# Optimization experiments

Measured on AMD Instinct MI355X. Metric: run time of the kernel, lower is better.

The kernel has to match this reference:

```python
import jax, jax.numpy as jnp
import numpy as np

B, N, E = 2, 20000, 200000
IN_F, OUT_F, HEADS = 256, 32, 4
NEG_SLOPE = 0.2


def setup_inputs() -> dict:
    key = jax.random.key(0)
    k1, k2, k3, k4 = jax.random.split(key, 4)
    x = jax.random.normal(k1, (B, N, IN_F), dtype=jnp.float32)
    edge_indices = jax.random.randint(k2, (2, E), 0, N, dtype=jnp.int64)
    # xavier-uniform-like scales
    W = jax.random.normal(k3, (OUT_F * HEADS, IN_F), dtype=jnp.float32) * np.float32(1.0 / np.sqrt(IN_F))
    a = jax.random.normal(k4, (2 * OUT_F, 1), dtype=jnp.float32) * np.float32(0.1)
    return {"x": x, "edge_indices": edge_indices, "W": W, "a": a}


def reference(x, edge_indices, W, a):
    Bq, Nq, _ = x.shape
    Hh, Ff = HEADS, OUT_F
    # h: [B, N, H, F]
    h = (x @ W.T).reshape(Bq, Nq, Hh, Ff)
    src, dst = edge_indices[0], edge_indices[1]
    Eq = src.shape[0]
    h_src = h[:, src]  # [B, E, H, F]
    h_dst = h[:, dst]  # [B, E, H, F]
    # scores = leaky_relu(concat(h_src, h_dst) @ a)  without materializing concat
    a_src, a_dst = a[:Ff, 0], a[Ff:, 0]
    scores = (jnp.einsum('behf,f->beh', h_src, a_src)
              + jnp.einsum('behf,f->beh', h_dst, a_dst))
    scores = jnp.where(scores > 0, scores, NEG_SLOPE * scores)  # LeakyReLU(0.2)
    # Original applies softmax over dim=0 (the BATCH dim) per edge
    sm = jax.nn.softmax(scores, axis=0)  # [B, E, H]
    # Original loop overwrites attention_weights[:, src] per edge, so only the
    # LAST edge with a given src survives.
    edge_ids = jnp.arange(Eq, dtype=jnp.int32)
    last_edge = jax.ops.segment_max(edge_ids, src, num_segments=Nq)
    has_edge = jax.ops.segment_sum(jnp.ones((Eq,), jnp.int32), src, num_segments=Nq) > 0
    last_edge = jnp.clip(last_edge, 0, Eq - 1)
    aw = jnp.where(has_edge[None, :, None], sm[:, last_edge], 0.0)  # [B, N, H]
    # aggregated[:, s] = aw[:, s] * sum_{edges i: src[i]==s} h_dst[:, i]
    seg = jax.ops.segment_sum(jnp.transpose(h_dst, (1, 0, 2, 3)), src, num_segments=Nq)  # [N,B,H,F]
    seg = jnp.transpose(seg, (1, 0, 2, 3))  # [B, N, H, F]
    aggregated = aw[..., None] * seg
    # mean over heads; dropout is identity in eval mode
    return aggregated.mean(axis=2)  # [B, N, F]
```

## Files before the change

kernel.cpp:

```cpp
#include <hip/hip_runtime.h>
#include <hip/hip_bf16.h>

#define BB 2
#define NN 20000
#define EE 200000
#define INF 256
#define OUTF 32
#define NH 4
#define HF 128
#define NEG_SLOPE 0.2f
#define GEMM_BLOCKS 625
#define EDGE_BLOCKS 782
#define CAP 96
#define OVF_CAP 8192

using bf16 = __hip_bfloat16;
typedef __attribute__((ext_vector_type(8))) short bf16x8;
typedef __attribute__((ext_vector_type(4))) float f32x4;

__device__ __forceinline__ float bf2f(unsigned short s){ return __uint_as_float((unsigned)s << 16); }
__device__ __forceinline__ ushort f2bf_bits(float f){
    __hip_bfloat16 b = __float2bfloat16(f);
    return *(ushort*)&b;
}

__device__ __forceinline__ int get_src(const int* ei, int e, int f64){
    return f64 ? ei[2 * e] : ei[e];
}
__device__ __forceinline__ int get_dst(const int* ei, int e, int f64){
    return f64 ? ei[2 * EE + 2 * e] : ei[EE + e];
}

__global__ void k_init(const ushort* __restrict__ xr, const int* __restrict__ er,
                       const void* __restrict__ Wv,
                       int* __restrict__ flags, ushort* __restrict__ wbf,
                       int* __restrict__ cnt, int* __restrict__ last_e,
                       int* __restrict__ ovf_cnt){
    int i = blockIdx.x * blockDim.x + threadIdx.x;
    if (i < NN){ cnt[i] = 0; last_e[i] = -1; }
    if (i == 0) *ovf_cnt = 0;
    if (blockIdx.x < 16){
        __shared__ int cnt_big, cnt_nz;
        if (threadIdx.x == 0){ cnt_big = 0; cnt_nz = 0; }
        __syncthreads();
        int big = 0;
        for (int k = threadIdx.x; k < 8192; k += blockDim.x){
            unsigned e = ((unsigned)xr[2 * k] >> 7) & 0xff;
            if (e >= 0xC0) big++;
        }
        int nz = 0;
        for (int k = threadIdx.x; k < 4096; k += blockDim.x){
            if (er[2 * k + 1] != 0) nz++;
        }
        atomicAdd(&cnt_big, big);
        atomicAdd(&cnt_nz, nz);
        __syncthreads();
        if (blockIdx.x == 0 && threadIdx.x == 0){
            flags[0] = (cnt_big >= 16) ? 1 : 0;
            flags[1] = (cnt_nz == 0) ? 1 : 0;
        }
        const bool f32w = (cnt_big >= 16);
        int fr = blockIdx.x * 256 + threadIdx.x;
        {
            int lane = fr & 63;
            int t    = (fr >> 6) & 3;
            int kc   = (fr >> 8) & 7;
            int ch   = fr >> 11;
            int col  = ch * 64 + t * 16 + (lane & 15);
            int kb   = kc * 32 + (lane >> 4) * 8;
            bf16x8 v;
            if (f32w){
                const float* wg = (const float*)Wv + (size_t)col * INF + kb;
                #pragma unroll
                for (int j = 0; j < 8; ++j) v[j] = (short)f2bf_bits(wg[j]);
            } else {
                const ushort* wg = (const ushort*)Wv + (size_t)col * INF + kb;
                #pragma unroll
                for (int j = 0; j < 8; ++j) v[j] = (short)wg[j];
            }
            *(bf16x8*)(wbf + (size_t)fr * 8) = v;
        }
    }
}

__global__ __launch_bounds__(256, 2)
void k_gemm(const void* __restrict__ xv_, const ushort* __restrict__ wbf,
            const void* __restrict__ av, const int* __restrict__ ei,
            const int* __restrict__ flags, ushort* __restrict__ h,
            float* __restrict__ alpha_s, float* __restrict__ alpha_d,
            int* __restrict__ last_e, int* __restrict__ cnt,
            ushort* __restrict__ slots, int* __restrict__ ovf_cnt,
            int* __restrict__ ovf_list){
    if (blockIdx.x < EDGE_BLOCKS){
        int f64 = flags[1];
        int e = blockIdx.x * 256 + threadIdx.x;
        if (e < EE){
            int s = get_src(ei, e, f64);
            int d = get_dst(ei, e, f64);
            atomicMax(&last_e[s], e);
            int idx = atomicAdd(&cnt[s], 1);
            if (idx < CAP) slots[(size_t)s * CAP + idx] = (ushort)d;
            else { int o = atomicAdd(ovf_cnt, 1); if (o < OVF_CAP) ovf_list[o] = e; }
        }
        return;
    }

    const int bid  = blockIdx.x - EDGE_BLOCKS;
    const int tid  = threadIdx.x;
    const int lane = tid & 63;
    const int w    = tid >> 6;
    const int l15  = lane & 15;
    const int q    = lane >> 4;
    const bool f32 = flags[0] != 0;

    const int row0 = bid * 64 + w * 16;

    f32x4 acc[2][4];
    #pragma unroll
    for (int c = 0; c < 2; ++c)
        #pragma unroll
        for (int t = 0; t < 4; ++t) acc[c][t] = (f32x4){0.f, 0.f, 0.f, 0.f};

    if (f32){
        const float* xp = (const float*)xv_ + (size_t)(row0 + l15) * INF + q * 8;
        float4 c0 = ((const float4*)xp)[0];
        float4 c1 = ((const float4*)xp)[1];
        #pragma unroll
        for (int kc = 0; kc < 8; ++kc){
            float4 n0, n1;
            if (kc < 7){
                const float4* p = (const float4*)(xp + (kc + 1) * 32);
                n0 = p[0];
                n1 = p[1];
            }
            bf16x8 afrag;
            afrag[0] = (short)f2bf_bits(c0.x); afrag[1] = (short)f2bf_bits(c0.y);
            afrag[2] = (short)f2bf_bits(c0.z); afrag[3] = (short)f2bf_bits(c0.w);
            afrag[4] = (short)f2bf_bits(c1.x); afrag[5] = (short)f2bf_bits(c1.y);
            afrag[6] = (short)f2bf_bits(c1.z); afrag[7] = (short)f2bf_bits(c1.w);
            #pragma unroll
            for (int c = 0; c < 2; ++c){
                const ushort* wb = wbf + (size_t)c * 16384;
                #pragma unroll
                for (int t = 0; t < 4; ++t){
                    bf16x8 bfrag = *(const bf16x8*)(wb + (((size_t)kc * 4 + t) * 64 + lane) * 8);
                    acc[c][t] = __builtin_amdgcn_mfma_f32_16x16x32_bf16(afrag, bfrag, acc[c][t], 0, 0, 0);
                }
            }
            if (kc < 7){ c0 = n0; c1 = n1; }
        }
    } else {
        const ushort* xp = (const ushort*)xv_ + (size_t)(row0 + l15) * INF + q * 8;
        bf16x8 af = *(const bf16x8*)xp;
        #pragma unroll
        for (int kc = 0; kc < 8; ++kc){
            bf16x8 nf;
            if (kc < 7) nf = *(const bf16x8*)(xp + (kc + 1) * 32);
            #pragma unroll
            for (int c = 0; c < 2; ++c){
                const ushort* wb = wbf + (size_t)c * 16384;
                #pragma unroll
                for (int t = 0; t < 4; ++t){
                    bf16x8 bfrag = *(const bf16x8*)(wb + (((size_t)kc * 4 + t) * 64 + lane) * 8);
                    acc[c][t] = __builtin_amdgcn_mfma_f32_16x16x32_bf16(af, bfrag, acc[c][t], 0, 0, 0);
                }
            }
            if (kc < 7) af = nf;
        }
    }

    #pragma unroll
    for (int r = 0; r < 4; ++r){
        int row = row0 + q * 4 + r;
        #pragma unroll
        for (int t = 0; t < 2; ++t){
            unsigned v0 = (unsigned)f2bf_bits(acc[0][t][r])
                        | ((unsigned)f2bf_bits(acc[0][t + 2][r]) << 16);
            unsigned v1 = (unsigned)f2bf_bits(acc[1][t][r])
                        | ((unsigned)f2bf_bits(acc[1][t + 2][r]) << 16);
            int f = t * 16 + l15;
            uint2 vv; vv.x = v0; vv.y = v1;
            *(uint2*)(h + (size_t)row * HF + f * 4) = vv;
        }
    }

    float as_lo, as_hi, ad_lo, ad_hi;
    if (f32){
        const float* af = (const float*)av;
        as_lo = af[l15];        as_hi = af[16 + l15];
        ad_lo = af[OUTF + l15]; ad_hi = af[OUTF + 16 + l15];
    } else {
        const ushort* ab = (const ushort*)av;
        as_lo = bf2f(ab[l15]);        as_hi = bf2f(ab[16 + l15]);
        ad_lo = bf2f(ab[OUTF + l15]); ad_hi = bf2f(ab[OUTF + 16 + l15]);
    }
    #pragma unroll
    for (int r = 0; r < 4; ++r){
        int row = row0 + q * 4 + r;
        #pragma unroll
        for (int c = 0; c < 2; ++c){
            #pragma unroll
            for (int hp = 0; hp < 2; ++hp){
                int t0 = hp * 2, t1 = hp * 2 + 1;
                float ps = acc[c][t0][r] * as_lo + acc[c][t1][r] * as_hi;
                float pd = acc[c][t0][r] * ad_lo + acc[c][t1][r] * ad_hi;
                ps += __shfl_down(ps, 8, 16); pd += __shfl_down(pd, 8, 16);
                ps += __shfl_down(ps, 4, 16); pd += __shfl_down(pd, 4, 16);
                ps += __shfl_down(ps, 2, 16); pd += __shfl_down(pd, 2, 16);
                ps += __shfl_down(ps, 1, 16); pd += __shfl_down(pd, 1, 16);
                if (l15 == 0){
                    size_t o = (size_t)row * NH + c * 2 + hp;
                    alpha_s[o] = ps;
                    alpha_d[o] = pd;
                }
            }
        }
    }
}

__global__ __launch_bounds__(256)
void k_agg(const ushort* __restrict__ slots, const int* __restrict__ cnt,
           const int* __restrict__ last_e, const int* __restrict__ ei,
           const int* __restrict__ flags,
           const float* __restrict__ alpha_s, const float* __restrict__ alpha_d,
           const ushort* __restrict__ h, float* __restrict__ aw,
           float* __restrict__ out_f){
    int lane = threadIdx.x & 63;
    int wid  = (blockIdx.x * blockDim.x + threadIdx.x) >> 6;
    int nw   = (gridDim.x * blockDim.x) >> 6;
    int b = lane >> 5;
    int f = lane & 31;
    int c  = lane & 7;
    int bb = c >> 2;
    int hh = c & 3;
    int f64 = flags[1];
    for (int n = wid; n < NN; n += nw){
        int m  = cnt[n]; if (m > CAP) m = CAP;
        int le = last_e[n];

        float my_aw = 0.f;
        if (le >= 0){
            int d = get_dst(ei, le, f64);
            float ss = alpha_s[((size_t)bb * NN + n) * NH + hh]
                     + alpha_d[((size_t)bb * NN + d) * NH + hh];
            float so = alpha_s[((size_t)(1 - bb) * NN + n) * NH + hh]
                     + alpha_d[((size_t)(1 - bb) * NN + d) * NH + hh];
            ss = ss > 0.f ? ss : NEG_SLOPE * ss;
            so = so > 0.f ? so : NEG_SLOPE * so;
            float mx = fmaxf(ss, so);
            float e0 = __expf(ss - mx);
            float e1 = __expf(so - mx);
            my_aw = 0.25f * e0 / (e0 + e1);
        }
        if (lane < 8) aw[((size_t)bb * NN + n) * NH + hh] = my_aw;

        float aw0 = __shfl(my_aw, (b << 2) + 0, 8);
        float aw1 = __shfl(my_aw, (b << 2) + 1, 8);
        float aw2 = __shfl(my_aw, (b << 2) + 2, 8);
        float aw3 = __shfl(my_aw, (b << 2) + 3, 8);

        const ushort* sl = slots + (size_t)n * CAP;
        const ushort* hb = h + (size_t)b * NN * HF + f * 4;
        float ax = 0.f, ay = 0.f, az = 0.f, aww = 0.f;
        int i = 0;
        for (; i + 4 <= m; i += 4){
            ushort4 dd = *(const ushort4*)(sl + i);
            ushort4 u0 = *(const ushort4*)(hb + (size_t)dd.x * HF);
            ushort4 u1 = *(const ushort4*)(hb + (size_t)dd.y * HF);
            ushort4 u2 = *(const ushort4*)(hb + (size_t)dd.z * HF);
            ushort4 u3 = *(const ushort4*)(hb + (size_t)dd.w * HF);
            ax += bf2f(u0.x) + bf2f(u1.x) + bf2f(u2.x) + bf2f(u3.x);
            ay += bf2f(u0.y) + bf2f(u1.y) + bf2f(u2.y) + bf2f(u3.y);
            az += bf2f(u0.z) + bf2f(u1.z) + bf2f(u2.z) + bf2f(u3.z);
            aww += bf2f(u0.w) + bf2f(u1.w) + bf2f(u2.w) + bf2f(u3.w);
        }
        for (; i < m; ++i){
            ushort4 u = *(const ushort4*)(hb + (size_t)sl[i] * HF);
            ax += bf2f(u.x); ay += bf2f(u.y); az += bf2f(u.z); aww += bf2f(u.w);
        }
        out_f[((size_t)b * NN + n) * OUTF + f] =
            aw0 * ax + aw1 * ay + aw2 * az + aw3 * aww;
    }
}

__global__ void k_fix(const int* __restrict__ ei, const int* __restrict__ flags,
                      const int* __restrict__ ovf_cnt, const int* __restrict__ ovf_list,
                      const ushort* __restrict__ h, const float* __restrict__ aw,
                      float* __restrict__ out_f){
    int lane = threadIdx.x & 63;
    int wid  = (blockIdx.x * blockDim.x + threadIdx.x) >> 6;
    int nw   = (gridDim.x * blockDim.x) >> 6;
    int b = lane >> 5;
    int f = lane & 31;
    int M = *ovf_cnt; if (M > OVF_CAP) M = OVF_CAP;
    int f64 = flags[1];
    for (int i = wid; i < M; i += nw){
        int e = ovf_list[i];
        int s = get_src(ei, e, f64);
        int d = get_dst(ei, e, f64);
        float4 awv = *(const float4*)(aw + ((size_t)b * NN + s) * NH);
        ushort4 u = *(const ushort4*)(h + ((size_t)b * NN + d) * HF + f * 4);
        float acc = awv.x * bf2f(u.x) + awv.y * bf2f(u.y)
                  + awv.z * bf2f(u.z) + awv.w * bf2f(u.w);
        atomicAdd(&out_f[((size_t)b * NN + s) * OUTF + f], acc);
    }
}

extern "C" void kernel_launch(void* const* d_in, const int* in_sizes, int n_in,
                              void* d_out, int out_size, void* d_ws, size_t ws_size,
                              hipStream_t stream){
    const void* x = d_in[0]; const void* eiv = d_in[1];
    const void* W = d_in[2]; const void* a  = d_in[3];
    for (int i = 0; i < n_in; ++i){
        if      (in_sizes[i] == BB * NN * INF) x   = d_in[i];
        else if (in_sizes[i] == 2 * EE)        eiv = d_in[i];
        else if (in_sizes[i] == HF * INF)      W   = d_in[i];
        else if (in_sizes[i] == 2 * OUTF)      a   = d_in[i];
    }
    const int* ei = (const int*)eiv;
    float* out = (float*)d_out;

    const size_t HN = (size_t)BB * NN * HF;
    char* p = (char*)d_ws;
    int*    flags    = (int*)p;                       p += 64;
    ushort* wbf      = (ushort*)p;                    p += 32768 * 2;
    ushort* h        = (ushort*)p;                    p += HN * 2;
    float*  alpha_s  = (float*)p;                     p += (size_t)BB * NN * NH * 4;
    float*  alpha_d  = (float*)p;                     p += (size_t)BB * NN * NH * 4;
    float*  aw       = (float*)p;                     p += (size_t)BB * NN * NH * 4;
    int*    last_e   = (int*)p;                       p += (size_t)NN * 4;
    int*    cnt      = (int*)p;                       p += (size_t)NN * 4;
    int*    ovf_cnt  = (int*)p;                       p += 64;
    int*    ovf_list = (int*)p;                       p += (size_t)OVF_CAP * 4;
    ushort* slots    = (ushort*)p;

    k_init <<<(NN + 255) / 256, 256, 0, stream>>>((const ushort*)x, ei, W, flags, wbf,
                                                  cnt, last_e, ovf_cnt);
    k_gemm <<<EDGE_BLOCKS + GEMM_BLOCKS, 256, 0, stream>>>(x, wbf, a, ei, flags, h,
                                                           alpha_s, alpha_d, last_e,
                                                           cnt, slots, ovf_cnt, ovf_list);
    k_agg  <<<2048, 256, 0, stream>>>(slots, cnt, last_e, ei, flags,
                                      alpha_s, alpha_d, h, aw, out);
    k_fix  <<<32, 256, 0, stream>>>(ei, flags, ovf_cnt, ovf_list, h, aw, out);
}
```

Before: 153.6 us.

## Store edge ids in slots and derive last edge during aggregation

```diff
diff --git a/kernel.cpp b/kernel.cpp
--- a/kernel.cpp
+++ b/kernel.cpp
@@ -11,7 +11,7 @@
 #define NEG_SLOPE 0.2f
 #define GEMM_BLOCKS 625
 #define EDGE_BLOCKS 782
-#define CAP 96
+#define CAP 48
 #define OVF_CAP 8192
 
 using bf16 = __hip_bfloat16;
@@ -89,18 +89,20 @@
             const int* __restrict__ flags, ushort* __restrict__ h,
             float* __restrict__ alpha_s, float* __restrict__ alpha_d,
             int* __restrict__ last_e, int* __restrict__ cnt,
-            ushort* __restrict__ slots, int* __restrict__ ovf_cnt,
+            unsigned* __restrict__ slots, int* __restrict__ ovf_cnt,
             int* __restrict__ ovf_list){
     if (blockIdx.x < EDGE_BLOCKS){
         int f64 = flags[1];
         int e = blockIdx.x * 256 + threadIdx.x;
         if (e < EE){
             int s = get_src(ei, e, f64);
-            int d = get_dst(ei, e, f64);
-            atomicMax(&last_e[s], e);
             int idx = atomicAdd(&cnt[s], 1);
-            if (idx < CAP) slots[(size_t)s * CAP + idx] = (ushort)d;
-            else { int o = atomicAdd(ovf_cnt, 1); if (o < OVF_CAP) ovf_list[o] = e; }
+            if (idx < CAP) slots[(size_t)s * CAP + idx] = (unsigned)e;
+            else {
+                atomicMax(&last_e[s], e);
+                int o = atomicAdd(ovf_cnt, 1);
+                if (o < OVF_CAP) ovf_list[o] = e;
+            }
         }
         return;
     }
@@ -219,7 +221,7 @@
 }
 
 __global__ __launch_bounds__(256)
-void k_agg(const ushort* __restrict__ slots, const int* __restrict__ cnt,
+void k_agg(const unsigned* __restrict__ slots, const int* __restrict__ cnt,
            const int* __restrict__ last_e, const int* __restrict__ ei,
            const int* __restrict__ flags,
            const float* __restrict__ alpha_s, const float* __restrict__ alpha_d,
@@ -238,6 +240,35 @@
         int m  = cnt[n]; if (m > CAP) m = CAP;
         int le = last_e[n];
 
+        const unsigned* sl = slots + (size_t)n * CAP;
+        const ushort* hb = h + (size_t)b * NN * HF + f * 4;
+        float ax = 0.f, ay = 0.f, az = 0.f, aww = 0.f;
+        int i = 0;
+        for (; i + 4 <= m; i += 4){
+            uint4 ee = *(const uint4*)(sl + i);
+            le = max(le, (int)ee.x); le = max(le, (int)ee.y);
+            le = max(le, (int)ee.z); le = max(le, (int)ee.w);
+            int d0 = get_dst(ei, (int)ee.x, f64);
+            int d1 = get_dst(ei, (int)ee.y, f64);
+            int d2 = get_dst(ei, (int)ee.z, f64);
+            int d3 = get_dst(ei, (int)ee.w, f64);
+            ushort4 u0 = *(const ushort4*)(hb + (size_t)d0 * HF);
+            ushort4 u1 = *(const ushort4*)(hb + (size_t)d1 * HF);
+            ushort4 u2 = *(const ushort4*)(hb + (size_t)d2 * HF);
+            ushort4 u3 = *(const ushort4*)(hb + (size_t)d3 * HF);
+            ax += bf2f(u0.x) + bf2f(u1.x) + bf2f(u2.x) + bf2f(u3.x);
+            ay += bf2f(u0.y) + bf2f(u1.y) + bf2f(u2.y) + bf2f(u3.y);
+            az += bf2f(u0.z) + bf2f(u1.z) + bf2f(u2.z) + bf2f(u3.z);
+            aww += bf2f(u0.w) + bf2f(u1.w) + bf2f(u2.w) + bf2f(u3.w);
+        }
+        for (; i < m; ++i){
+            int e = (int)sl[i];
+            le = max(le, e);
+            int d = get_dst(ei, e, f64);
+            ushort4 u = *(const ushort4*)(hb + (size_t)d * HF);
+            ax += bf2f(u.x); ay += bf2f(u.y); az += bf2f(u.z); aww += bf2f(u.w);
+        }
+
         float my_aw = 0.f;
         if (le >= 0){
             int d = get_dst(ei, le, f64);
@@ -259,25 +290,6 @@
         float aw2 = __shfl(my_aw, (b << 2) + 2, 8);
         float aw3 = __shfl(my_aw, (b << 2) + 3, 8);
 
-        const ushort* sl = slots + (size_t)n * CAP;
-        const ushort* hb = h + (size_t)b * NN * HF + f * 4;
-        float ax = 0.f, ay = 0.f, az = 0.f, aww = 0.f;
-        int i = 0;
-        for (; i + 4 <= m; i += 4){
-            ushort4 dd = *(const ushort4*)(sl + i);
-            ushort4 u0 = *(const ushort4*)(hb + (size_t)dd.x * HF);
-            ushort4 u1 = *(const ushort4*)(hb + (size_t)dd.y * HF);
-            ushort4 u2 = *(const ushort4*)(hb + (size_t)dd.z * HF);
-            ushort4 u3 = *(const ushort4*)(hb + (size_t)dd.w * HF);
-            ax += bf2f(u0.x) + bf2f(u1.x) + bf2f(u2.x) + bf2f(u3.x);
-            ay += bf2f(u0.y) + bf2f(u1.y) + bf2f(u2.y) + bf2f(u3.y);
-            az += bf2f(u0.z) + bf2f(u1.z) + bf2f(u2.z) + bf2f(u3.z);
-            aww += bf2f(u0.w) + bf2f(u1.w) + bf2f(u2.w) + bf2f(u3.w);
-        }
-        for (; i < m; ++i){
-            ushort4 u = *(const ushort4*)(hb + (size_t)sl[i] * HF);
-            ax += bf2f(u.x); ay += bf2f(u.y); az += bf2f(u.z); aww += bf2f(u.w);
-        }
         out_f[((size_t)b * NN + n) * OUTF + f] =
             aw0 * ax + aw1 * ay + aw2 * az + aw3 * aww;
     }
@@ -322,17 +334,17 @@
 
     const size_t HN = (size_t)BB * NN * HF;
     char* p = (char*)d_ws;
-    int*    flags    = (int*)p;                       p += 64;
-    ushort* wbf      = (ushort*)p;                    p += 32768 * 2;
-    ushort* h        = (ushort*)p;                    p += HN * 2;
-    float*  alpha_s  = (float*)p;                     p += (size_t)BB * NN * NH * 4;
-    float*  alpha_d  = (float*)p;                     p += (size_t)BB * NN * NH * 4;
-    float*  aw       = (float*)p;                     p += (size_t)BB * NN * NH * 4;
-    int*    last_e   = (int*)p;                       p += (size_t)NN * 4;
-    int*    cnt      = (int*)p;                       p += (size_t)NN * 4;
-    int*    ovf_cnt  = (int*)p;                       p += 64;
-    int*    ovf_list = (int*)p;                       p += (size_t)OVF_CAP * 4;
-    ushort* slots    = (ushort*)p;
+    int*      flags    = (int*)p;                     p += 64;
+    ushort*   wbf      = (ushort*)p;                  p += 32768 * 2;
+    ushort*   h        = (ushort*)p;                  p += HN * 2;
+    float*    alpha_s  = (float*)p;                   p += (size_t)BB * NN * NH * 4;
+    float*    alpha_d  = (float*)p;                   p += (size_t)BB * NN * NH * 4;
+    float*    aw       = (float*)p;                   p += (size_t)BB * NN * NH * 4;
+    int*      last_e   = (int*)p;                     p += (size_t)NN * 4;
+    int*      cnt      = (int*)p;                     p += (size_t)NN * 4;
+    int*      ovf_cnt  = (int*)p;                     p += 64;
+    int*      ovf_list = (int*)p;                     p += (size_t)OVF_CAP * 4;
+    unsigned* slots    = (unsigned*)p;
 
     k_init <<<(NN + 255) / 256, 256, 0, stream>>>((const ushort*)x, ei, W, flags, wbf,
                                                   cnt, last_e, ovf_cnt);
```

Result: no change. 152.3 us (-0.8%).

## Interleave batch rows of h, pack edge id into slots, split edge kernel

Applied to the files above, without the earlier changes.

```diff
diff --git a/kernel.cpp b/kernel.cpp
--- a/kernel.cpp
+++ b/kernel.cpp
@@ -8,15 +8,17 @@
 #define OUTF 32
 #define NH 4
 #define HF 128
+#define HF2 256
 #define NEG_SLOPE 0.2f
 #define GEMM_BLOCKS 625
 #define EDGE_BLOCKS 782
-#define CAP 96
+#define CAP 48
 #define OVF_CAP 8192
 
 using bf16 = __hip_bfloat16;
 typedef __attribute__((ext_vector_type(8))) short bf16x8;
 typedef __attribute__((ext_vector_type(4))) float f32x4;
+typedef unsigned long long u64;
 
 __device__ __forceinline__ float bf2f(unsigned short s){ return __uint_as_float((unsigned)s << 16); }
 __device__ __forceinline__ ushort f2bf_bits(float f){
@@ -31,13 +33,17 @@
     return f64 ? ei[2 * EE + 2 * e] : ei[EE + e];
 }
 
+__device__ __forceinline__ size_t hrow_of(int row){
+    return (row >= NN) ? ((size_t)(row - NN) * 2 + 1) : ((size_t)row * 2);
+}
+
 __global__ void k_init(const ushort* __restrict__ xr, const int* __restrict__ er,
                        const void* __restrict__ Wv,
                        int* __restrict__ flags, ushort* __restrict__ wbf,
-                       int* __restrict__ cnt, int* __restrict__ last_e,
+                       int* __restrict__ cnt, u64* __restrict__ last_e64,
                        int* __restrict__ ovf_cnt){
     int i = blockIdx.x * blockDim.x + threadIdx.x;
-    if (i < NN){ cnt[i] = 0; last_e[i] = -1; }
+    if (i < NN){ cnt[i] = 0; last_e64[i] = 0ULL; }
     if (i == 0) *ovf_cnt = 0;
     if (blockIdx.x < 16){
         __shared__ int cnt_big, cnt_nz;
@@ -83,29 +89,33 @@
     }
 }
 
+__global__ __launch_bounds__(256)
+void k_edge(const int* __restrict__ ei, const int* __restrict__ flags,
+            int* __restrict__ cnt, u64* __restrict__ slots,
+            u64* __restrict__ last_e64, int* __restrict__ ovf_cnt,
+            int* __restrict__ ovf_list){
+    int f64 = flags[1];
+    int e = blockIdx.x * 256 + threadIdx.x;
+    if (e < EE){
+        int s = get_src(ei, e, f64);
+        int d = get_dst(ei, e, f64);
+        u64 pk = ((u64)(unsigned)(e + 1) << 16) | (unsigned)(d & 0xFFFF);
+        int idx = atomicAdd(&cnt[s], 1);
+        if (idx < CAP) slots[(size_t)s * CAP + idx] = pk;
+        else {
+            atomicMax(&last_e64[s], pk);
+            int o = atomicAdd(ovf_cnt, 1);
+            if (o < OVF_CAP) ovf_list[o] = e;
+        }
+    }
+}
+
 __global__ __launch_bounds__(256, 2)
 void k_gemm(const void* __restrict__ xv_, const ushort* __restrict__ wbf,
-            const void* __restrict__ av, const int* __restrict__ ei,
-            const int* __restrict__ flags, ushort* __restrict__ h,
-            float* __restrict__ alpha_s, float* __restrict__ alpha_d,
-            int* __restrict__ last_e, int* __restrict__ cnt,
-            ushort* __restrict__ slots, int* __restrict__ ovf_cnt,
-            int* __restrict__ ovf_list){
-    if (blockIdx.x < EDGE_BLOCKS){
-        int f64 = flags[1];
-        int e = blockIdx.x * 256 + threadIdx.x;
-        if (e < EE){
-            int s = get_src(ei, e, f64);
-            int d = get_dst(ei, e, f64);
-            atomicMax(&last_e[s], e);
-            int idx = atomicAdd(&cnt[s], 1);
-            if (idx < CAP) slots[(size_t)s * CAP + idx] = (ushort)d;
-            else { int o = atomicAdd(ovf_cnt, 1); if (o < OVF_CAP) ovf_list[o] = e; }
-        }
-        return;
-    }
-
-    const int bid  = blockIdx.x - EDGE_BLOCKS;
+            const void* __restrict__ av, const int* __restrict__ flags,
+            ushort* __restrict__ h,
+            float* __restrict__ alpha_s, float* __restrict__ alpha_d){
+    const int bid  = blockIdx.x;
     const int tid  = threadIdx.x;
     const int lane = tid & 63;
     const int w    = tid >> 6;
@@ -172,6 +182,7 @@
     #pragma unroll
     for (int r = 0; r < 4; ++r){
         int row = row0 + q * 4 + r;
+        ushort* hp_ = h + hrow_of(row) * HF;
         #pragma unroll
         for (int t = 0; t < 2; ++t){
             unsigned v0 = (unsigned)f2bf_bits(acc[0][t][r])
@@ -180,7 +191,7 @@
                         | ((unsigned)f2bf_bits(acc[1][t + 2][r]) << 16);
             int f = t * 16 + l15;
             uint2 vv; vv.x = v0; vv.y = v1;
-            *(uint2*)(h + (size_t)row * HF + f * 4) = vv;
+            *(uint2*)(hp_ + f * 4) = vv;
         }
     }
 
@@ -219,9 +230,8 @@
 }
 
 __global__ __launch_bounds__(256)
-void k_agg(const ushort* __restrict__ slots, const int* __restrict__ cnt,
-           const int* __restrict__ last_e, const int* __restrict__ ei,
-           const int* __restrict__ flags,
+void k_agg(const u64* __restrict__ slots, const int* __restrict__ cnt,
+           const u64* __restrict__ last_e64,
            const float* __restrict__ alpha_s, const float* __restrict__ alpha_d,
            const ushort* __restrict__ h, float* __restrict__ aw,
            float* __restrict__ out_f){
@@ -233,14 +243,43 @@
     int c  = lane & 7;
     int bb = c >> 2;
     int hh = c & 3;
-    int f64 = flags[1];
+    const ushort* hb = h + b * HF + f * 4;
     for (int n = wid; n < NN; n += nw){
-        int m  = cnt[n]; if (m > CAP) m = CAP;
-        int le = last_e[n];
+        int m = cnt[n]; if (m > CAP) m = CAP;
+        u64 le = last_e64[n];
+
+        const u64* sl = slots + (size_t)n * CAP;
+        float ax = 0.f, ay = 0.f, az = 0.f, aww = 0.f;
+        int i = 0;
+        for (; i + 4 <= m; i += 4){
+            ulonglong2 p0 = *(const ulonglong2*)(sl + i);
+            ulonglong2 p1 = *(const ulonglong2*)(sl + i + 2);
+            le = p0.x > le ? p0.x : le;  le = p0.y > le ? p0.y : le;
+            le = p1.x > le ? p1.x : le;  le = p1.y > le ? p1.y : le;
+            int d0 = (int)(p0.x & 0xFFFFULL);
+            int d1 = (int)(p0.y & 0xFFFFULL);
+            int d2 = (int)(p1.x & 0xFFFFULL);
+            int d3 = (int)(p1.y & 0xFFFFULL);
+            ushort4 u0 = *(const ushort4*)(hb + (size_t)d0 * HF2);
+            ushort4 u1 = *(const ushort4*)(hb + (size_t)d1 * HF2);
+            ushort4 u2 = *(const ushort4*)(hb + (size_t)d2 * HF2);
+            ushort4 u3 = *(const ushort4*)(hb + (size_t)d3 * HF2);
+            ax += bf2f(u0.x) + bf2f(u1.x) + bf2f(u2.x) + bf2f(u3.x);
+            ay += bf2f(u0.y) + bf2f(u1.y) + bf2f(u2.y) + bf2f(u3.y);
+            az += bf2f(u0.z) + bf2f(u1.z) + bf2f(u2.z) + bf2f(u3.z);
+            aww += bf2f(u0.w) + bf2f(u1.w) + bf2f(u2.w) + bf2f(u3.w);
+        }
+        for (; i < m; ++i){
+            u64 pk = sl[i];
+            le = pk > le ? pk : le;
+            int d = (int)(pk & 0xFFFFULL);
+            ushort4 u = *(const ushort4*)(hb + (size_t)d * HF2);
+            ax += bf2f(u.x); ay += bf2f(u.y); az += bf2f(u.z); aww += bf2f(u.w);
+        }
 
         float my_aw = 0.f;
-        if (le >= 0){
-            int d = get_dst(ei, le, f64);
+        if (le != 0ULL){
+            int d = (int)(le & 0xFFFFULL);
             float ss = alpha_s[((size_t)bb * NN + n) * NH + hh]
                      + alpha_d[((size_t)bb * NN + d) * NH + hh];
             float so = alpha_s[((size_t)(1 - bb) * NN + n) * NH + hh]
@@ -259,25 +298,6 @@
         float aw2 = __shfl(my_aw, (b << 2) + 2, 8);
         float aw3 = __shfl(my_aw, (b << 2) + 3, 8);
 
-        const ushort* sl = slots + (size_t)n * CAP;
-        const ushort* hb = h + (size_t)b * NN * HF + f * 4;
-        float ax = 0.f, ay = 0.f, az = 0.f, aww = 0.f;
-        int i = 0;
-        for (; i + 4 <= m; i += 4){
-            ushort4 dd = *(const ushort4*)(sl + i);
-            ushort4 u0 = *(const ushort4*)(hb + (size_t)dd.x * HF);
-            ushort4 u1 = *(const ushort4*)(hb + (size_t)dd.y * HF);
-            ushort4 u2 = *(const ushort4*)(hb + (size_t)dd.z * HF);
-            ushort4 u3 = *(const ushort4*)(hb + (size_t)dd.w * HF);
-            ax += bf2f(u0.x) + bf2f(u1.x) + bf2f(u2.x) + bf2f(u3.x);
-            ay += bf2f(u0.y) + bf2f(u1.y) + bf2f(u2.y) + bf2f(u3.y);
-            az += bf2f(u0.z) + bf2f(u1.z) + bf2f(u2.z) + bf2f(u3.z);
-            aww += bf2f(u0.w) + bf2f(u1.w) + bf2f(u2.w) + bf2f(u3.w);
-        }
-        for (; i < m; ++i){
-            ushort4 u = *(const ushort4*)(hb + (size_t)sl[i] * HF);
-            ax += bf2f(u.x); ay += bf2f(u.y); az += bf2f(u.z); aww += bf2f(u.w);
-        }
         out_f[((size_t)b * NN + n) * OUTF + f] =
             aw0 * ax + aw1 * ay + aw2 * az + aw3 * aww;
     }
@@ -299,7 +319,7 @@
         int s = get_src(ei, e, f64);
         int d = get_dst(ei, e, f64);
         float4 awv = *(const float4*)(aw + ((size_t)b * NN + s) * NH);
-        ushort4 u = *(const ushort4*)(h + ((size_t)b * NN + d) * HF + f * 4);
+        ushort4 u = *(const ushort4*)(h + ((size_t)d * 2 + b) * HF + f * 4);
         float acc = awv.x * bf2f(u.x) + awv.y * bf2f(u.y)
                   + awv.z * bf2f(u.z) + awv.w * bf2f(u.w);
         atomicAdd(&out_f[((size_t)b * NN + s) * OUTF + f], acc);
@@ -322,24 +342,24 @@
 
     const size_t HN = (size_t)BB * NN * HF;
     char* p = (char*)d_ws;
-    int*    flags    = (int*)p;                       p += 64;
-    ushort* wbf      = (ushort*)p;                    p += 32768 * 2;
-    ushort* h        = (ushort*)p;                    p += HN * 2;
-    float*  alpha_s  = (float*)p;                     p += (size_t)BB * NN * NH * 4;
-    float*  alpha_d  = (float*)p;                     p += (size_t)BB * NN * NH * 4;
-    float*  aw       = (float*)p;                     p += (size_t)BB * NN * NH * 4;
-    int*    last_e   = (int*)p;                       p += (size_t)NN * 4;
-    int*    cnt      = (int*)p;                       p += (size_t)NN * 4;
-    int*    ovf_cnt  = (int*)p;                       p += 64;
-    int*    ovf_list = (int*)p;                       p += (size_t)OVF_CAP * 4;
-    ushort* slots    = (ushort*)p;
+    int*   flags    = (int*)p;                        p += 64;
+    ushort* wbf     = (ushort*)p;                     p += 32768 * 2;
+    ushort* h       = (ushort*)p;                     p += HN * 2;
+    float* alpha_s  = (float*)p;                      p += (size_t)BB * NN * NH * 4;
+    float* alpha_d  = (float*)p;                      p += (size_t)BB * NN * NH * 4;
+    float* aw       = (float*)p;                      p += (size_t)BB * NN * NH * 4;
+    u64*   last_e64 = (u64*)p;                        p += (size_t)NN * 8;
+    int*   cnt      = (int*)p;                        p += (size_t)NN * 4;
+    int*   ovf_cnt  = (int*)p;                        p += 64;
+    int*   ovf_list = (int*)p;                        p += (size_t)OVF_CAP * 4;
+    u64*   slots    = (u64*)p;
 
     k_init <<<(NN + 255) / 256, 256, 0, stream>>>((const ushort*)x, ei, W, flags, wbf,
-                                                  cnt, last_e, ovf_cnt);
-    k_gemm <<<EDGE_BLOCKS + GEMM_BLOCKS, 256, 0, stream>>>(x, wbf, a, ei, flags, h,
-                                                           alpha_s, alpha_d, last_e,
-                                                           cnt, slots, ovf_cnt, ovf_list);
-    k_agg  <<<2048, 256, 0, stream>>>(slots, cnt, last_e, ei, flags,
-                                      alpha_s, alpha_d, h, aw, out);
+                                                  cnt, last_e64, ovf_cnt);
+    k_edge <<<EDGE_BLOCKS, 256, 0, stream>>>(ei, flags, cnt, slots, last_e64,
+                                             ovf_cnt, ovf_list);
+    k_gemm <<<GEMM_BLOCKS, 256, 0, stream>>>(x, wbf, a, flags, h, alpha_s, alpha_d);
+    k_agg  <<<2048, 256, 0, stream>>>(slots, cnt, last_e64, alpha_s, alpha_d,
+                                      h, aw, out);
     k_fix  <<<32, 256, 0, stream>>>(ei, flags, ovf_cnt, ovf_list, h, aw, out);
 }
```

After: 146.2 us. 4.8% less time.
